# Kernel tuning notes

Measured on AMD Instinct MI355X. Metric: run time of the kernel, lower is better.

Reference implementation:

```python
import jax, jax.numpy as jnp
import numpy as np
from jax import lax

EPS = 1e-5
N_TCN = 24  # 3 repeats * 8 layers
DILATIONS = [2 ** (i % 8) for i in range(N_TCN)]


def conv1d(x, w, stride=1, padding=0, dilation=1, groups=1):
    # x: (N, C, T), w: (O, I//g, K)
    return lax.conv_general_dilated(
        x, w, window_strides=(stride,), padding=[(padding, padding)],
        rhs_dilation=(dilation,), dimension_numbers=('NCH', 'OIH', 'NCH'),
        feature_group_count=groups)


def ste_sign(w):
    # forward: sign(w); backward: identity
    return lax.stop_gradient(jnp.sign(w) - w) + w


def bit_conv1d(x, w, scale, stride=1, padding=0, dilation=1, groups=1):
    x_scale = jnp.clip(jnp.mean(jnp.abs(x), axis=(1, 2), keepdims=True), EPS)
    w_scale = jnp.mean(jnp.abs(w))
    out = conv1d(x / x_scale, ste_sign(w), stride, padding, dilation, groups)
    return out * w_scale * x_scale * scale


def bit_linear(x, w, b, scale):
    x_scale = jnp.clip(jnp.mean(jnp.abs(x), axis=-1, keepdims=True), EPS)
    w_scale = jnp.mean(jnp.abs(w))
    out = (x / x_scale) @ ste_sign(w).T + b
    return out * w_scale * x_scale * scale


def group_norm1(x, gamma, beta):
    # GroupNorm(1, C): normalize over (C, T) per sample
    m = jnp.mean(x, axis=(1, 2), keepdims=True)
    v = jnp.var(x, axis=(1, 2), keepdims=True)
    xn = (x - m) * lax.rsqrt(v + EPS)
    return xn * gamma[None, :, None] + beta[None, :, None]


def prelu(x, a):
    return jnp.where(x >= 0, x, a * x)


def setup_inputs() -> dict:
    key = jax.random.key(0)
    ks = jax.random.split(key, 12)
    B, T = 16, 64000
    E, Bn, C, H = 512, 256, 512, 256
    return {
        'x': jax.random.normal(ks[0], (B, 1, T), jnp.float32),
        'enc_w': jax.random.normal(ks[1], (E, 1, 40), jnp.float32) * 0.05,
        'enc_gamma': jnp.ones((E,), jnp.float32),
        'enc_beta': jnp.zeros((E,), jnp.float32),
        'enc_prelu': jnp.float32(0.25),
        'bn_w': jax.random.normal(ks[2], (Bn, E, 1), jnp.float32),
        'bn_scale': jnp.ones((1,), jnp.float32),
        'ti_w': jax.random.normal(ks[3], (C, Bn, 1), jnp.float32),
        'ti_scale': jnp.ones((1,), jnp.float32),
        'dw_w': jax.random.normal(ks[4], (N_TCN, C, 1, 3), jnp.float32) * 0.1,
        'pw_w': jax.random.normal(ks[5], (N_TCN, C, C, 1), jnp.float32),
        'pw_scale': jnp.ones((N_TCN, 1), jnp.float32),
        'tcn_gamma': jnp.ones((N_TCN, C), jnp.float32),
        'tcn_beta': jnp.zeros((N_TCN, C), jnp.float32),
        'tcn_prelu': jnp.full((N_TCN,), 0.25, jnp.float32),
        'fc1_w': jax.random.normal(ks[6], (H, C), jnp.float32),
        'fc1_b': jnp.zeros((H,), jnp.float32),
        'fc1_scale': jnp.ones((1,), jnp.float32),
        'head_prelu': jnp.float32(0.25),
        'fco_w': jax.random.normal(ks[7], (1, H), jnp.float32),
        'fco_b': jnp.zeros((1,), jnp.float32),
        'fco_scale': jnp.ones((1,), jnp.float32),
    }


def reference(x, enc_w, enc_gamma, enc_beta, enc_prelu, bn_w, bn_scale,
              ti_w, ti_scale, dw_w, pw_w, pw_scale, tcn_gamma, tcn_beta,
              tcn_prelu, fc1_w, fc1_b, fc1_scale, head_prelu,
              fco_w, fco_b, fco_scale):
    # AudioEncoder: conv(k=40, s=20, p=20) -> GroupNorm(1) -> PReLU
    f = conv1d(x, enc_w, stride=20, padding=20)
    f = prelu(group_norm1(f, enc_gamma, enc_beta), enc_prelu)
    # bottleneck / tcn_input 1x1 BitConv1d
    f = bit_conv1d(f, bn_w, bn_scale)
    f = bit_conv1d(f, ti_w, ti_scale)
    # 24 depthwise-separable TCN layers with dilations 2^(i%8)
    C = f.shape[1]
    for i in range(N_TCN):
        d = DILATIONS[i]
        res = f
        out = conv1d(f, dw_w[i], padding=d, dilation=d, groups=C)
        out = prelu(group_norm1(out, tcn_gamma[i], tcn_beta[i]), tcn_prelu[i])
        out = bit_conv1d(out, pw_w[i], pw_scale[i])
        f = out + res
    # head: global average pool -> BitLinear -> PReLU -> BitLinear -> sigmoid
    h = jnp.mean(f, axis=-1)  # (B, C)
    h = prelu(bit_linear(h, fc1_w, fc1_b, fc1_scale), head_prelu)
    score = jax.nn.sigmoid(bit_linear(h, fco_w, fco_b, fco_scale))
    return score
```

## Files before the change

kernel.cpp:

```cpp
#include <hip/hip_runtime.h>
#include <hip/hip_bf16.h>
#include <math.h>


#define EPSF 1e-5f

constexpr int B_   = 16;
constexpr int TIN  = 64000;
constexpr int TOUT = 3201;
constexpr int TPAD = 3328;
constexpr int E_   = 512;
constexpr int BNC  = 256;
constexpr int C_   = 512;
constexpr int NT   = 24;
constexpr int H_   = 256;
constexpr int NM   = TPAD / 128;
constexpr int NM64 = TPAD / 64;

#define FL_GN    2
#define FL_RES   8

typedef __attribute__((ext_vector_type(8))) short short8;
typedef __attribute__((ext_vector_type(4))) float floatx4;

__device__ __forceinline__ float b2f(short s) {
    unsigned u = ((unsigned)(unsigned short)s) << 16;
    float f; __builtin_memcpy(&f, &u, 4); return f;
}
__device__ __forceinline__ short f2b(float f) {
    __hip_bfloat16 h = __float2bfloat16(f);
    short s; __builtin_memcpy(&s, &h, 2); return s;
}
__device__ __forceinline__ short f2b_fast(float f) {
    unsigned u; __builtin_memcpy(&u, &f, 4);
    return (short)((u + 0x8000u) >> 16);
}
__device__ __forceinline__ short bsign(float w) {
    return (w > 0.f) ? (short)0x3F80 : ((w < 0.f) ? (short)0xBF80 : (short)0);
}
__device__ __forceinline__ float fsign(float w) {
    return (w > 0.f) ? 1.f : ((w < 0.f) ? -1.f : 0.f);
}

__device__ float blockReduceSum(float v, float* red, int nw) {
    __syncthreads();
    int lane = threadIdx.x & 63, wid = threadIdx.x >> 6;
#pragma unroll
    for (int o = 32; o > 0; o >>= 1) v += __shfl_down(v, o, 64);
    if (lane == 0) red[wid] = v;
    __syncthreads();
    if (threadIdx.x == 0) {
        float s = 0.f;
        for (int i = 0; i < nw; ++i) s += red[i];
        red[0] = s;
    }
    __syncthreads();
    return red[0];
}

__global__ void k_signcvt(const float* __restrict__ src,
                          __hip_bfloat16* __restrict__ dst, int n) {
    int i = (blockIdx.x * 256 + threadIdx.x) * 8;
    if (i >= n) return;
    float4 a = *(const float4*)(src + i);
    float4 c = *(const float4*)(src + i + 4);
    short8 v;
    v[0]=bsign(a.x); v[1]=bsign(a.y); v[2]=bsign(a.z); v[3]=bsign(a.w);
    v[4]=bsign(c.x); v[5]=bsign(c.y); v[6]=bsign(c.z); v[7]=bsign(c.w);
    *(short8*)(dst + i) = v;
}

__global__ void k_encw(const float* __restrict__ src,
                       __hip_bfloat16* __restrict__ dst) {
    int id = blockIdx.x * 256 + threadIdx.x;
    int r = id >> 3, cc = id & 7;
    short8 v = (short8){0,0,0,0,0,0,0,0};
    if (cc < 5) {
        const float* s = src + r * 40 + cc * 8;
#pragma unroll
        for (int e = 0; e < 8; ++e) v[e] = f2b(s[e]);
    }
    *(short8*)(dst + r * 64 + cc * 8) = v;
}

__global__ void k_absmean(const float* __restrict__ p, int n, int slice_stride,
                          float* __restrict__ out) {
    __shared__ float red[8];
    const float* q = p + (size_t)blockIdx.y * (size_t)slice_stride;
    float s = 0.f;
    for (int i = blockIdx.x * blockDim.x + threadIdx.x; i < n;
         i += gridDim.x * blockDim.x)
        s += fabsf(q[i]);
    s = blockReduceSum(s, red, 4);
    if (threadIdx.x == 0) atomicAdd(out + blockIdx.y, s);
}

template <int FLAGS>
__global__ __launch_bounds__(256, 3) void k_gemm(
    const __hip_bfloat16* __restrict__ Aact,
    const __hip_bfloat16* __restrict__ Bw, __hip_bfloat16* __restrict__ Yout,
    const __hip_bfloat16* __restrict__ Res,
    const float* __restrict__ gnstats, const float* __restrict__ gamma,
    const float* __restrict__ beta, const float* __restrict__ prelu, float invN,
    const float* __restrict__ wsum, float inv_nw, const float* __restrict__ scale,
    int K, int N, int nnshift) {
    __shared__ __align__(16) short As[64 * 64];
    __shared__ __align__(16) short Bs[256 * 64];

    int tid = threadIdx.x;
    int gid = blockIdx.x;
    int xcd = gid & 7, grp = gid >> 3;
    int nidx = grp & ((1 << nnshift) - 1);
    int mb = (grp >> nnshift) * 8 + xcd;
    int m0 = (mb % NM64) * 64;
    int b  = mb / NM64;
    int n0 = nidx * 256;

    int lane = tid & 63, wn = tid >> 6;
    int l15 = lane & 15, quad = lane >> 4;

    float mean = 0.f, ginv = 1.f, pr = 0.f;
    if (FLAGS & FL_GN) {
        float s0 = gnstats[b * 2], s1 = gnstats[b * 2 + 1];
        mean = s0 * invN;
        float var  = s1 * invN - mean * mean;
        ginv = rsqrtf(var + EPSF);
        pr = prelu[0];
    }

    floatx4 acc[4][4];
#pragma unroll
    for (int i = 0; i < 4; ++i)
#pragma unroll
        for (int j = 0; j < 4; ++j) acc[i][j] = (floatx4){0.f, 0.f, 0.f, 0.f};

    short8 ra[2], rb[8];
    int r0 = tid >> 3, cc = tid & 7;
    int nk = K >> 6;

    auto loadRaw = [&](int kt) {
        int k0 = kt * 64;
#pragma unroll
        for (int j = 0; j < 2; ++j)
            ra[j] = *(const short8*)(Aact +
                ((size_t)b * TPAD + m0 + j * 32 + r0) * K + k0 + cc * 8);
#pragma unroll
        for (int j = 0; j < 8; ++j)
            rb[j] = *(const short8*)(Bw + (size_t)(n0 + j * 32 + r0) * K
                                     + k0 + cc * 8);
    };

    auto xform = [&](int kt) {
        if (!(FLAGS & FL_GN)) return;
        int k = kt * 64 + cc * 8;
        float4 g0 = *(const float4*)(gamma + k);
        float4 g1 = *(const float4*)(gamma + k + 4);
        float4 b0 = *(const float4*)(beta + k);
        float4 b1 = *(const float4*)(beta + k + 4);
        float gs[8] = {g0.x,g0.y,g0.z,g0.w,g1.x,g1.y,g1.z,g1.w};
        float bs[8] = {b0.x,b0.y,b0.z,b0.w,b1.x,b1.y,b1.z,b1.w};
        float sc[8], sh[8];
#pragma unroll
        for (int e = 0; e < 8; ++e) {
            sc[e] = gs[e] * ginv;
            sh[e] = bs[e] - mean * sc[e];
        }
#pragma unroll
        for (int j = 0; j < 2; ++j) {
            if (m0 + j * 32 + r0 < TOUT) {
                short8 v = ra[j];
#pragma unroll
                for (int e = 0; e < 8; ++e) {
                    float f = b2f(v[e]) * sc[e] + sh[e];
                    f = fmaxf(f, 0.f) + pr * fminf(f, 0.f);
                    v[e] = f2b_fast(f);
                }
                ra[j] = v;
            } else {
                ra[j] = (short8){0,0,0,0,0,0,0,0};
            }
        }
    };

    int sw = (cc ^ (r0 & 7)) * 8;
    loadRaw(0);
    xform(0);
    for (int kt = 0; kt < nk; ++kt) {
        __syncthreads();
#pragma unroll
        for (int j = 0; j < 2; ++j)
            *(short8*)&As[(j * 32 + r0) * 64 + sw] = ra[j];
#pragma unroll
        for (int j = 0; j < 8; ++j)
            *(short8*)&Bs[(j * 32 + r0) * 64 + sw] = rb[j];
        __syncthreads();
        if (kt + 1 < nk) loadRaw(kt + 1);
#pragma unroll
        for (int s = 0; s < 2; ++s) {
            short8 af[4], bf[4];
#pragma unroll
            for (int i = 0; i < 4; ++i) {
                int row = i * 16 + l15;
                int ch = (s * 4 + quad) ^ (row & 7);
                af[i] = *(const short8*)&As[row * 64 + ch * 8];
            }
#pragma unroll
            for (int j = 0; j < 4; ++j) {
                int row = wn * 64 + j * 16 + l15;
                int ch = (s * 4 + quad) ^ (row & 7);
                bf[j] = *(const short8*)&Bs[row * 64 + ch * 8];
            }
#pragma unroll
            for (int i = 0; i < 4; ++i)
#pragma unroll
                for (int j = 0; j < 4; ++j)
                    acc[i][j] = __builtin_amdgcn_mfma_f32_16x16x32_bf16(
                        af[i], bf[j], acc[i][j], 0, 0, 0);
        }
        if (kt + 1 < nk) xform(kt + 1);
    }

    float alpha = wsum[0] * inv_nw * scale[0];
#pragma unroll
    for (int i = 0; i < 4; ++i) {
#pragma unroll
        for (int j = 0; j < 4; ++j) {
            int tb = m0 + i * 16 + quad * 4;
            int n  = n0 + wn * 64 + j * 16 + l15;
#pragma unroll
            for (int r = 0; r < 4; ++r) {
                int t = tb + r;
                float v = alpha * acc[i][j][r];
                size_t off = ((size_t)b * TPAD + t) * N + n;
                if (FLAGS & FL_RES) v += b2f(*(const short*)(Res + off));
                *(short*)(Yout + off) = f2b_fast(v);
            }
        }
    }
}

__global__ __launch_bounds__(512) void k_gemm_enc(
    const float* __restrict__ xraw, const __hip_bfloat16* __restrict__ Bw,
    __hip_bfloat16* __restrict__ Yout, float* __restrict__ statsOut) {
    __shared__ __align__(16) short As[128 * 64];
    __shared__ __align__(16) short Bs[256 * 64];
    __shared__ float red[8];

    int tid = threadIdx.x;
    int gid = blockIdx.x;
    int xcd = gid & 7, grp = gid >> 3;
    int nidx = grp & 1;
    int mb = (grp >> 1) * 8 + xcd;
    int m0 = (mb % NM) * 128;
    int b  = mb / NM;
    int n0 = nidx * 256;

    int lane = tid & 63, wid = tid >> 6;
    int wm = wid >> 2, wn = wid & 3;
    int l15 = lane & 15, quad = lane >> 4;

    floatx4 acc[4][4];
#pragma unroll
    for (int i = 0; i < 4; ++i)
#pragma unroll
        for (int j = 0; j < 4; ++j) acc[i][j] = (floatx4){0.f, 0.f, 0.f, 0.f};

    int r0 = tid >> 3, cc = tid & 7;
    int sw = (cc ^ (r0 & 7)) * 8;
    const float* xp = xraw + (size_t)b * TIN;

#pragma unroll
    for (int j = 0; j < 2; ++j) {
        int t = m0 + j * 64 + r0;
        short8 v = (short8){0,0,0,0,0,0,0,0};
        if (t < TOUT && cc < 5) {
            int base = 20 * t + cc * 8 - 20;
            if (base >= 0 && base + 8 <= TIN) {
                float4 x0 = *(const float4*)(xp + base);
                float4 x1 = *(const float4*)(xp + base + 4);
                v[0]=f2b(x0.x); v[1]=f2b(x0.y); v[2]=f2b(x0.z); v[3]=f2b(x0.w);
                v[4]=f2b(x1.x); v[5]=f2b(x1.y); v[6]=f2b(x1.z); v[7]=f2b(x1.w);
            } else {
#pragma unroll
                for (int e = 0; e < 8; ++e) {
                    int xi = base + e;
                    if (xi >= 0 && xi < TIN) v[e] = f2b(xp[xi]);
                }
            }
        }
        *(short8*)&As[(j * 64 + r0) * 64 + sw] = v;
    }
#pragma unroll
    for (int j = 0; j < 4; ++j)
        *(short8*)&Bs[(j * 64 + r0) * 64 + sw] =
            *(const short8*)(Bw + (size_t)(n0 + j * 64 + r0) * 64 + cc * 8);
    __syncthreads();
#pragma unroll
    for (int s = 0; s < 2; ++s) {
        short8 af[4], bf[4];
#pragma unroll
        for (int i = 0; i < 4; ++i) {
            int row = wm * 64 + i * 16 + l15;
            int ch = (s * 4 + quad) ^ (row & 7);
            af[i] = *(const short8*)&As[row * 64 + ch * 8];
        }
#pragma unroll
        for (int j = 0; j < 4; ++j) {
            int row = wn * 64 + j * 16 + l15;
            int ch = (s * 4 + quad) ^ (row & 7);
            bf[j] = *(const short8*)&Bs[row * 64 + ch * 8];
        }
#pragma unroll
        for (int i = 0; i < 4; ++i)
#pragma unroll
            for (int j = 0; j < 4; ++j)
                acc[i][j] = __builtin_amdgcn_mfma_f32_16x16x32_bf16(
                    af[i], bf[j], acc[i][j], 0, 0, 0);
    }

    float ls = 0.f, lq = 0.f;
#pragma unroll
    for (int i = 0; i < 4; ++i) {
#pragma unroll
        for (int j = 0; j < 4; ++j) {
            int tb = m0 + wm * 64 + i * 16 + quad * 4;
            int n  = n0 + wn * 64 + j * 16 + l15;
#pragma unroll
            for (int r = 0; r < 4; ++r) {
                int t = tb + r;
                float v = acc[i][j][r];
                *(short*)(Yout + ((size_t)b * TPAD + t) * E_ + n) = f2b_fast(v);
                if (t < TOUT) { ls += v; lq += v * v; }
            }
        }
    }
    ls = blockReduceSum(ls, red, 8);
    lq = blockReduceSum(lq, red, 8);
    if (tid == 0) {
        atomicAdd(statsOut + b * 2, ls);
        atomicAdd(statsOut + b * 2 + 1, lq);
    }
}

__global__ __launch_bounds__(256) void k_dwconv(
    const __hip_bfloat16* __restrict__ trunk, const float* __restrict__ w,
    __hip_bfloat16* __restrict__ act, float* __restrict__ stats, int d) {
    __shared__ float red[8];
    int b = blockIdx.y, t0 = blockIdx.x * 128;
    int tid = threadIdx.x, lane = tid & 63, wv = tid >> 6;
    int c8 = lane * 8;
    float wr[24];
    const float4* wp4 = (const float4*)(w + c8 * 3);
#pragma unroll
    for (int q = 0; q < 6; ++q) ((float4*)wr)[q] = wp4[q];
    const __hip_bfloat16* base = trunk + (size_t)b * TPAD * C_;
    __hip_bfloat16* ob = act + (size_t)b * TPAD * C_;
    float ls = 0.f, lq = 0.f;
    for (int it = 0; it < 32; ++it) {
        int t = t0 + it * 4 + wv;
        if (t < TOUT) {
            short8 mid = *(const short8*)(base + (size_t)t * C_ + c8);
            short8 prv = (t >= d) ? *(const short8*)(base + (size_t)(t - d) * C_ + c8)
                                  : (short8){0,0,0,0,0,0,0,0};
            short8 nxt = (t + d < TPAD) ? *(const short8*)(base + (size_t)(t + d) * C_ + c8)
                                        : (short8){0,0,0,0,0,0,0,0};
            short8 o;
#pragma unroll
            for (int e = 0; e < 8; ++e) {
                float v = wr[e * 3 + 1] * b2f(mid[e])
                        + wr[e * 3 + 0] * b2f(prv[e])
                        + wr[e * 3 + 2] * b2f(nxt[e]);
                o[e] = f2b_fast(v); ls += v; lq += v * v;
            }
            *(short8*)(ob + (size_t)t * C_ + c8) = o;
        } else {
            *(short8*)(ob + (size_t)t * C_ + c8) = (short8){0,0,0,0,0,0,0,0};
        }
    }
    ls = blockReduceSum(ls, red, 4);
    lq = blockReduceSum(lq, red, 4);
    if (tid == 0) {
        atomicAdd(stats + b * 2, ls);
        atomicAdd(stats + b * 2 + 1, lq);
    }
}

__global__ void k_tmean(const __hip_bfloat16* __restrict__ trunk,
                        float* __restrict__ h0) {
    int b = blockIdx.y, t0 = blockIdx.x * 128;
    int tid = threadIdx.x;
    const __hip_bfloat16* base = trunk + (size_t)b * TPAD * C_;
    float s0 = 0.f, s1 = 0.f;
    for (int it = 0; it < 128; ++it) {
        int t = t0 + it;
        if (t >= TOUT) break;
        s0 += b2f(*(const short*)(base + (size_t)t * C_ + tid));
        s1 += b2f(*(const short*)(base + (size_t)t * C_ + tid + 256));
    }
    atomicAdd(h0 + b * C_ + tid, s0);
    atomicAdd(h0 + b * C_ + tid + 256, s1);
}

__global__ void k_head(const float* __restrict__ h0,
                       const float* __restrict__ fc1_w, const float* __restrict__ fc1_b,
                       const float* __restrict__ fc1_scale, const float* __restrict__ head_prelu,
                       const float* __restrict__ fco_w, const float* __restrict__ fco_b,
                       const float* __restrict__ fco_scale,
                       const float* __restrict__ wsums, float* __restrict__ out) {
    __shared__ float sh0[512];
    __shared__ float red[8];
    int b = blockIdx.x, tid = threadIdx.x;
    sh0[tid]       = h0[b * C_ + tid] / (float)TOUT;
    sh0[tid + 256] = h0[b * C_ + 256 + tid] / (float)TOUT;
    __syncthreads();
    float av = fabsf(sh0[tid]) + fabsf(sh0[tid + 256]);
    float xs1 = blockReduceSum(av, red, 4) / 512.f;
    xs1 = fmaxf(xs1, EPSF);
    float ws1 = wsums[26] / 131072.f;
    float sc1 = fc1_scale[0];
    const float* wrow = fc1_w + tid * 512;
    float s = 0.f;
    for (int c = 0; c < 512; ++c) s += sh0[c] * fsign(wrow[c]);
    float h1 = s * ws1 * sc1 + fc1_b[tid] * ws1 * xs1 * sc1;
    float a = head_prelu[0];
    h1 = (h1 >= 0.f) ? h1 : a * h1;
    float xs2 = blockReduceSum(fabsf(h1), red, 4) / 256.f;
    xs2 = fmaxf(xs2, EPSF);
    float zpart = h1 * fsign(fco_w[tid]);
    float z = blockReduceSum(zpart, red, 4);
    if (tid == 0) {
        float ws2 = wsums[27] / 256.f;
        float sc2 = fco_scale[0];
        z = z * ws2 * sc2 + fco_b[0] * ws2 * xs2 * sc2;
        out[b] = 1.f / (1.f + expf(-z));
    }
}

extern "C" void kernel_launch(void* const* d_in, const int* in_sizes, int n_in,
                              void* d_out, int out_size, void* d_ws, size_t ws_size,
                              hipStream_t stream) {
    const float* x        = (const float*)d_in[0];
    const float* enc_w    = (const float*)d_in[1];
    const float* enc_g    = (const float*)d_in[2];
    const float* enc_be   = (const float*)d_in[3];
    const float* enc_pr   = (const float*)d_in[4];
    const float* bn_w     = (const float*)d_in[5];
    const float* bn_scale = (const float*)d_in[6];
    const float* ti_w     = (const float*)d_in[7];
    const float* ti_scale = (const float*)d_in[8];
    const float* dw_w     = (const float*)d_in[9];
    const float* pw_w     = (const float*)d_in[10];
    const float* pw_scale = (const float*)d_in[11];
    const float* tg       = (const float*)d_in[12];
    const float* tb       = (const float*)d_in[13];
    const float* tp       = (const float*)d_in[14];
    const float* fc1_w    = (const float*)d_in[15];
    const float* fc1_b    = (const float*)d_in[16];
    const float* fc1_s    = (const float*)d_in[17];
    const float* head_pr  = (const float*)d_in[18];
    const float* fco_w    = (const float*)d_in[19];
    const float* fco_b    = (const float*)d_in[20];
    const float* fco_s    = (const float*)d_in[21];
    float* out = (float*)d_out;

    char* ws = (char*)d_ws;
    size_t fmapH = (size_t)B_ * TPAD * C_ * sizeof(__hip_bfloat16);
    __hip_bfloat16* trunk = (__hip_bfloat16*)ws;
    __hip_bfloat16* act   = (__hip_bfloat16*)(ws + fmapH);
    __hip_bfloat16* xe    = (__hip_bfloat16*)(ws + 2 * fmapH);
    __hip_bfloat16* wenc  = (__hip_bfloat16*)(ws + 3 * fmapH);
    __hip_bfloat16* wbn   = wenc + 512 * 64;
    __hip_bfloat16* wti   = wbn + 256 * 512;
    __hip_bfloat16* wpw   = wti + 512 * 256;
    float* stats = (float*)(wpw + (size_t)NT * 512 * 512);
    float* wsums = stats + 800;
    float* h0    = stats + 832;

    hipMemsetAsync(stats, 0, (832 + B_ * C_) * sizeof(float), stream);

    k_encw<<<16, 256, 0, stream>>>(enc_w, wenc);
    k_signcvt<<<(256 * 512) / 2048, 256, 0, stream>>>(bn_w, wbn, 256 * 512);
    k_signcvt<<<(512 * 256) / 2048, 256, 0, stream>>>(ti_w, wti, 512 * 256);
    k_signcvt<<<(NT * 512 * 512) / 2048, 256, 0, stream>>>(pw_w, wpw, NT * 512 * 512);

    k_absmean<<<dim3(8, 1),  256, 0, stream>>>(bn_w,  BNC * C_, 0,        wsums + 0);
    k_absmean<<<dim3(8, 1),  256, 0, stream>>>(ti_w,  C_ * BNC, 0,        wsums + 1);
    k_absmean<<<dim3(8, NT), 256, 0, stream>>>(pw_w,  C_ * C_,  C_ * C_,  wsums + 2);
    k_absmean<<<dim3(8, 1),  256, 0, stream>>>(fc1_w, H_ * C_,  0,        wsums + 26);
    k_absmean<<<dim3(1, 1),  256, 0, stream>>>(fco_w, H_,       0,        wsums + 27);

    float invGN = 1.f / ((float)C_ * TOUT);

    k_gemm_enc<<<NM * B_ * 2, 512, 0, stream>>>(x, wenc, xe, stats);

    k_gemm<FL_GN><<<NM64 * B_, 256, 0, stream>>>(
        xe, wbn, act, nullptr,
        stats, enc_g, enc_be, enc_pr, invGN,
        wsums + 0, 1.f / (BNC * C_), bn_scale,
        E_, BNC, 0);

    k_gemm<0><<<NM64 * B_ * 2, 256, 0, stream>>>(
        act, wti, trunk, nullptr,
        nullptr, nullptr, nullptr, nullptr, 0.f,
        wsums + 1, 1.f / (C_ * BNC), ti_scale,
        BNC, C_, 1);

    for (int i = 0; i < NT; ++i) {
        int d = 1 << (i & 7);
        float* st = stats + (1 + i) * 32;
        k_dwconv<<<dim3(NM, B_), 256, 0, stream>>>(
            trunk, dw_w + (size_t)i * C_ * 3, act, st, d);
        k_gemm<FL_GN | FL_RES><<<NM64 * B_ * 2, 256, 0, stream>>>(
            act, wpw + (size_t)i * C_ * C_, trunk, trunk,
            st, tg + i * C_, tb + i * C_, tp + i, invGN,
            wsums + 2 + i, 1.f / (C_ * C_), pw_scale + i,
            C_, C_, 1);
    }

    k_tmean<<<dim3(NM, B_), 256, 0, stream>>>(trunk, h0);
    k_head<<<B_, 256, 0, stream>>>(h0, fc1_w, fc1_b, fc1_s, head_pr,
                                   fco_w, fco_b, fco_s, wsums, out);
}
```

Measured before the change: 2.672 ms.

## Fuse depthwise conv into pointwise GEMM prologue with ping-pong trunk buffers

```diff
diff --git a/kernel.cpp b/kernel.cpp
--- a/kernel.cpp
+++ b/kernel.cpp
@@ -19,6 +19,7 @@
 
 #define FL_GN    2
 #define FL_RES   8
+#define FL_DW    32
 
 typedef __attribute__((ext_vector_type(8))) short short8;
 typedef __attribute__((ext_vector_type(4))) float floatx4;
@@ -102,6 +103,7 @@
     const __hip_bfloat16* __restrict__ Res,
     const float* __restrict__ gnstats, const float* __restrict__ gamma,
     const float* __restrict__ beta, const float* __restrict__ prelu, float invN,
+    const float* __restrict__ dwW, int d,
     const float* __restrict__ wsum, float inv_nw, const float* __restrict__ scale,
     int K, int N, int nnshift) {
     __shared__ __align__(16) short As[64 * 64];
@@ -134,16 +136,33 @@
 #pragma unroll
         for (int j = 0; j < 4; ++j) acc[i][j] = (floatx4){0.f, 0.f, 0.f, 0.f};
 
-    short8 ra[2], rb[8];
+    constexpr int NRA = (FLAGS & FL_DW) ? 6 : 2;
+    short8 ra[NRA], rb[8];
     int r0 = tid >> 3, cc = tid & 7;
     int nk = K >> 6;
 
     auto loadRaw = [&](int kt) {
         int k0 = kt * 64;
-#pragma unroll
-        for (int j = 0; j < 2; ++j)
-            ra[j] = *(const short8*)(Aact +
-                ((size_t)b * TPAD + m0 + j * 32 + r0) * K + k0 + cc * 8);
+        if (FLAGS & FL_DW) {
+#pragma unroll
+            for (int j = 0; j < 2; ++j) {
+                int t = m0 + j * 32 + r0;
+                const __hip_bfloat16* rm = Aact +
+                    ((size_t)b * TPAD + t) * K + k0 + cc * 8;
+                ra[j * 3 + 1] = *(const short8*)rm;
+                ra[j * 3 + 0] = (t >= d)
+                    ? *(const short8*)(rm - (size_t)d * K)
+                    : (short8){0,0,0,0,0,0,0,0};
+                ra[j * 3 + 2] = (t + d < TPAD)
+                    ? *(const short8*)(rm + (size_t)d * K)
+                    : (short8){0,0,0,0,0,0,0,0};
+            }
+        } else {
+#pragma unroll
+            for (int j = 0; j < 2; ++j)
+                ra[j] = *(const short8*)(Aact +
+                    ((size_t)b * TPAD + m0 + j * 32 + r0) * K + k0 + cc * 8);
+        }
 #pragma unroll
         for (int j = 0; j < 8; ++j)
             rb[j] = *(const short8*)(Bw + (size_t)(n0 + j * 32 + r0) * K
@@ -165,19 +184,39 @@
             sc[e] = gs[e] * ginv;
             sh[e] = bs[e] - mean * sc[e];
         }
+        float wv[24];
+        if (FLAGS & FL_DW) {
+            const float* wp = dwW + (size_t)k * 3;
+#pragma unroll
+            for (int q = 0; q < 6; ++q) ((float4*)wv)[q] = *(const float4*)(wp + q * 4);
+        }
 #pragma unroll
         for (int j = 0; j < 2; ++j) {
             if (m0 + j * 32 + r0 < TOUT) {
-                short8 v = ra[j];
-#pragma unroll
-                for (int e = 0; e < 8; ++e) {
-                    float f = b2f(v[e]) * sc[e] + sh[e];
-                    f = fmaxf(f, 0.f) + pr * fminf(f, 0.f);
-                    v[e] = f2b_fast(f);
+                short8 v;
+                if (FLAGS & FL_DW) {
+                    short8 p = ra[j * 3 + 0], m = ra[j * 3 + 1], nx = ra[j * 3 + 2];
+#pragma unroll
+                    for (int e = 0; e < 8; ++e) {
+                        float f = wv[e * 3 + 1] * b2f(m[e])
+                                + wv[e * 3 + 0] * b2f(p[e])
+                                + wv[e * 3 + 2] * b2f(nx[e]);
+                        f = f * sc[e] + sh[e];
+                        f = fmaxf(f, 0.f) + pr * fminf(f, 0.f);
+                        v[e] = f2b_fast(f);
+                    }
+                } else {
+                    v = ra[j];
+#pragma unroll
+                    for (int e = 0; e < 8; ++e) {
+                        float f = b2f(v[e]) * sc[e] + sh[e];
+                        f = fmaxf(f, 0.f) + pr * fminf(f, 0.f);
+                        v[e] = f2b_fast(f);
+                    }
                 }
-                ra[j] = v;
+                ra[j * (NRA / 2)] = v;
             } else {
-                ra[j] = (short8){0,0,0,0,0,0,0,0};
+                ra[j * (NRA / 2)] = (short8){0,0,0,0,0,0,0,0};
             }
         }
     };
@@ -189,7 +228,7 @@
         __syncthreads();
 #pragma unroll
         for (int j = 0; j < 2; ++j)
-            *(short8*)&As[(j * 32 + r0) * 64 + sw] = ra[j];
+            *(short8*)&As[(j * 32 + r0) * 64 + sw] = ra[j * (NRA / 2)];
 #pragma unroll
         for (int j = 0; j < 8; ++j)
             *(short8*)&Bs[(j * 32 + r0) * 64 + sw] = rb[j];
@@ -342,9 +381,9 @@
     }
 }
 
-__global__ __launch_bounds__(256) void k_dwconv(
+__global__ __launch_bounds__(256) void k_dwstats(
     const __hip_bfloat16* __restrict__ trunk, const float* __restrict__ w,
-    __hip_bfloat16* __restrict__ act, float* __restrict__ stats, int d) {
+    float* __restrict__ stats, int d) {
     __shared__ float red[8];
     int b = blockIdx.y, t0 = blockIdx.x * 128;
     int tid = threadIdx.x, lane = tid & 63, wv = tid >> 6;
@@ -354,7 +393,6 @@
 #pragma unroll
     for (int q = 0; q < 6; ++q) ((float4*)wr)[q] = wp4[q];
     const __hip_bfloat16* base = trunk + (size_t)b * TPAD * C_;
-    __hip_bfloat16* ob = act + (size_t)b * TPAD * C_;
     float ls = 0.f, lq = 0.f;
     for (int it = 0; it < 32; ++it) {
         int t = t0 + it * 4 + wv;
@@ -364,17 +402,13 @@
                                   : (short8){0,0,0,0,0,0,0,0};
             short8 nxt = (t + d < TPAD) ? *(const short8*)(base + (size_t)(t + d) * C_ + c8)
                                         : (short8){0,0,0,0,0,0,0,0};
-            short8 o;
 #pragma unroll
             for (int e = 0; e < 8; ++e) {
                 float v = wr[e * 3 + 1] * b2f(mid[e])
                         + wr[e * 3 + 0] * b2f(prv[e])
                         + wr[e * 3 + 2] * b2f(nxt[e]);
-                o[e] = f2b_fast(v); ls += v; lq += v * v;
-            }
-            *(short8*)(ob + (size_t)t * C_ + c8) = o;
-        } else {
-            *(short8*)(ob + (size_t)t * C_ + c8) = (short8){0,0,0,0,0,0,0,0};
+                ls += v; lq += v * v;
+            }
         }
     }
     ls = blockReduceSum(ls, red, 4);
@@ -465,9 +499,10 @@
 
     char* ws = (char*)d_ws;
     size_t fmapH = (size_t)B_ * TPAD * C_ * sizeof(__hip_bfloat16);
-    __hip_bfloat16* trunk = (__hip_bfloat16*)ws;
-    __hip_bfloat16* act   = (__hip_bfloat16*)(ws + fmapH);
-    __hip_bfloat16* xe    = (__hip_bfloat16*)(ws + 2 * fmapH);
+    __hip_bfloat16* trunk0 = (__hip_bfloat16*)ws;
+    __hip_bfloat16* act    = (__hip_bfloat16*)(ws + fmapH);
+    __hip_bfloat16* trunk1 = (__hip_bfloat16*)(ws + 2 * fmapH);
+    __hip_bfloat16* xe     = trunk1;
     __hip_bfloat16* wenc  = (__hip_bfloat16*)(ws + 3 * fmapH);
     __hip_bfloat16* wbn   = wenc + 512 * 64;
     __hip_bfloat16* wti   = wbn + 256 * 512;
@@ -496,28 +531,34 @@
     k_gemm<FL_GN><<<NM64 * B_, 256, 0, stream>>>(
         xe, wbn, act, nullptr,
         stats, enc_g, enc_be, enc_pr, invGN,
+        nullptr, 0,
         wsums + 0, 1.f / (BNC * C_), bn_scale,
         E_, BNC, 0);
 
     k_gemm<0><<<NM64 * B_ * 2, 256, 0, stream>>>(
-        act, wti, trunk, nullptr,
+        act, wti, trunk0, nullptr,
         nullptr, nullptr, nullptr, nullptr, 0.f,
+        nullptr, 0,
         wsums + 1, 1.f / (C_ * BNC), ti_scale,
         BNC, C_, 1);
 
+    __hip_bfloat16* ping[2] = {trunk0, trunk1};
     for (int i = 0; i < NT; ++i) {
         int d = 1 << (i & 7);
         float* st = stats + (1 + i) * 32;
-        k_dwconv<<<dim3(NM, B_), 256, 0, stream>>>(
-            trunk, dw_w + (size_t)i * C_ * 3, act, st, d);
-        k_gemm<FL_GN | FL_RES><<<NM64 * B_ * 2, 256, 0, stream>>>(
-            act, wpw + (size_t)i * C_ * C_, trunk, trunk,
+        __hip_bfloat16* tin  = ping[i & 1];
+        __hip_bfloat16* tout = ping[(i + 1) & 1];
+        k_dwstats<<<dim3(NM, B_), 256, 0, stream>>>(
+            tin, dw_w + (size_t)i * C_ * 3, st, d);
+        k_gemm<FL_DW | FL_GN | FL_RES><<<NM64 * B_ * 2, 256, 0, stream>>>(
+            tin, wpw + (size_t)i * C_ * C_, tout, tin,
             st, tg + i * C_, tb + i * C_, tp + i, invGN,
+            dw_w + (size_t)i * C_ * 3, d,
             wsums + 2 + i, 1.f / (C_ * C_), pw_scale + i,
             C_, C_, 1);
     }
 
-    k_tmean<<<dim3(NM, B_), 256, 0, stream>>>(trunk, h0);
+    k_tmean<<<dim3(NM, B_), 256, 0, stream>>>(ping[0], h0);
     k_head<<<B_, 256, 0, stream>>>(h0, fc1_w, fc1_b, fc1_s, head_pr,
                                    fco_w, fco_b, fco_s, wsums, out);
 }
```

Measured after the change: 8.789 ms. 229% more time.
